# Kernel tuning notes

Hardware: AMD Instinct MI355X
Metric: run time of the kernel (lower is better)

## Reference

```python
import jax, jax.numpy as jnp
import numpy as np

HEAD_SIZE = 128

def setup_inputs() -> dict:
    key = jax.random.key(0)
    ks = jax.random.split(key, 4)
    B, T, C, H = 8, 2048, 1024, HEAD_SIZE
    x = jax.random.normal(ks[0], (B, T, C), dtype=jnp.float32)
    Wk = jax.random.normal(ks[1], (C, H), dtype=jnp.float32) * (C ** -0.5)
    Wq = jax.random.normal(ks[2], (C, H), dtype=jnp.float32) * (C ** -0.5)
    Wv = jax.random.normal(ks[3], (C, H), dtype=jnp.float32) * (C ** -0.5)
    return {"x": x, "Wk": Wk, "Wq": Wq, "Wv": Wv}

def reference(x, Wk, Wq, Wv):
    # x: [B,T,C]; projections to [B,T,H]
    k = jnp.einsum('btc,ch->bth', x, Wk)
    q = jnp.einsum('btc,ch->bth', x, Wq)
    v = jnp.einsum('btc,ch->bth', x, Wv)
    scale = HEAD_SIZE ** -0.5
    wei = jnp.einsum('bqh,bkh->bqk', q, k) * scale  # [B,T,T]
    T = x.shape[1]
    causal = jnp.tril(jnp.ones((T, T), dtype=bool))
    wei = jnp.where(causal, wei, -jnp.inf)
    wei = jax.nn.softmax(wei, axis=-1)
    # dropout p=0 (eval) -> identity
    out = jnp.einsum('bqk,bkh->bqh', wei, v)  # [B,T,H]
    return out
```

## Files before the change

### kernel.cpp

```cpp
#include <hip/hip_runtime.h>

#define B_DIM 8
#define T_DIM 2048
#define C_DIM 1024
#define H_DIM 128

typedef __attribute__((ext_vector_type(8))) short bf16x8;
typedef __attribute__((ext_vector_type(4))) float f32x4;

__device__ __forceinline__ short f2bf(float f) {
  union { float f; unsigned u; } v; v.f = f;
  unsigned u = v.u;
  unsigned r = (u + 0x7FFFu + ((u >> 16) & 1u)) >> 16;
  return (short)r;
}

__device__ __forceinline__ void gload_lds16(const short* g, short* l) {
  __builtin_amdgcn_global_load_lds(
      (const __attribute__((address_space(1))) void*)g,
      (__attribute__((address_space(3))) void*)l, 16, 0, 0);
}

__device__ __forceinline__ float rowmax16(float x) {
  union { float f; int i; } a, t;
  a.f = x;
  t.i = __builtin_amdgcn_update_dpp(a.i, a.i, 0x128, 0xf, 0xf, false);
  a.f = fmaxf(a.f, t.f);
  t.i = __builtin_amdgcn_update_dpp(a.i, a.i, 0x124, 0xf, 0xf, false);
  a.f = fmaxf(a.f, t.f);
  t.i = __builtin_amdgcn_update_dpp(a.i, a.i, 0x122, 0xf, 0xf, false);
  a.f = fmaxf(a.f, t.f);
  t.i = __builtin_amdgcn_update_dpp(a.i, a.i, 0x121, 0xf, 0xf, false);
  a.f = fmaxf(a.f, t.f);
  return a.f;
}
__device__ __forceinline__ float rowsum16(float x) {
  union { float f; int i; } a, t;
  a.f = x;
  t.i = __builtin_amdgcn_update_dpp(a.i, a.i, 0x128, 0xf, 0xf, false);
  a.f += t.f;
  t.i = __builtin_amdgcn_update_dpp(a.i, a.i, 0x124, 0xf, 0xf, false);
  a.f += t.f;
  t.i = __builtin_amdgcn_update_dpp(a.i, a.i, 0x122, 0xf, 0xf, false);
  a.f += t.f;
  t.i = __builtin_amdgcn_update_dpp(a.i, a.i, 0x121, 0xf, 0xf, false);
  a.f += t.f;
  return a.f;
}

#define NWE ((3 * C_DIM * H_DIM) / 8)

__global__ __launch_bounds__(256) void wprep_kernel(
    const float* __restrict__ Wk, const float* __restrict__ Wq,
    const float* __restrict__ Wv, short* __restrict__ Wt) {
  int j = blockIdx.x * 256 + threadIdx.x;
  if (j >= NWE) return;
  int w = j >> 14;
  int r = j & 16383;
  int h = r >> 7;
  int c0 = (r & 127) * 8;
  const float* W = (w == 0) ? Wk : ((w == 1) ? Wq : Wv);
  __attribute__((aligned(16))) short t[8];
#pragma unroll
  for (int i = 0; i < 8; i++) t[i] = f2bf(W[(size_t)(c0 + i) * H_DIM + h]);
  *(int4*)(Wt + (size_t)w * (C_DIM * H_DIM) + h * C_DIM + c0) = *(const int4*)t;
}

__global__ __launch_bounds__(512, 2) void projf_kernel(
    const float* __restrict__ x, const short* __restrict__ Wt,
    short* __restrict__ Kp, short* __restrict__ Qb, short* __restrict__ Vp) {
  const int m0 = blockIdx.x * 64;
  __shared__ short As[64][72];
  __shared__ short Bs[384 * 64];
  const int tid  = threadIdx.x;
  const int lane = tid & 63;
  const int wv   = tid >> 6;
  const int n    = lane & 15;
  const int quad = lane >> 4;
  const int mh = wv >> 2;
  const int nq = wv & 3;

  const int ar = tid >> 3, ac = (tid & 7) * 8;
  const float* xrow = x + (size_t)(m0 + ar) * C_DIM + ac;
  const int brl = lane >> 3;
  const int bce = 8 * ((lane & 7) ^ brl);

  f32x4 acc[2][6];
#pragma unroll
  for (int i = 0; i < 2; i++)
#pragma unroll
    for (int j = 0; j < 6; j++) {
      f32x4 z = {0.f, 0.f, 0.f, 0.f};
      acc[i][j] = z;
    }

  float4 ax0, ax1;
  auto LOADA = [&](int k0) {
    ax0 = *(const float4*)(xrow + k0);
    ax1 = *(const float4*)(xrow + k0 + 4);
  };
  auto STOREA = [&]() {
    __attribute__((aligned(16))) short t8[8];
    t8[0] = f2bf(ax0.x); t8[1] = f2bf(ax0.y); t8[2] = f2bf(ax0.z); t8[3] = f2bf(ax0.w);
    t8[4] = f2bf(ax1.x); t8[5] = f2bf(ax1.y); t8[6] = f2bf(ax1.z); t8[7] = f2bf(ax1.w);
    *(int4*)&As[ar][ac] = *(const int4*)t8;
  };

  LOADA(0);
  for (int it = 0; it < 16; it++) {
    const int k0 = it * 64;
    __syncthreads();
#pragma unroll
    for (int h = 0; h < 6; h++) {
      int c = wv * 6 + h;
      gload_lds16(Wt + (size_t)(c * 8 + brl) * C_DIM + k0 + bce, &Bs[c * 512]);
    }
    STOREA();
    if (it < 15) LOADA(k0 + 64);
    __syncthreads();

#pragma unroll
    for (int kk = 0; kk < 2; kk++) {
      bf16x8 aF[2], bF[6];
#pragma unroll
      for (int mt = 0; mt < 2; mt++)
        aF[mt] = *(const bf16x8*)&As[mh * 32 + mt * 16 + n][kk * 32 + quad * 8];
#pragma unroll
      for (int nt = 0; nt < 6; nt++) {
        int row = nq * 96 + nt * 16 + n;
        int off = (kk * 64 + quad * 16) ^ ((row & 7) << 4);
        bF[nt] = *(const bf16x8*)((const char*)&Bs[row * 64] + off);
      }
#pragma unroll
      for (int mt = 0; mt < 2; mt++)
#pragma unroll
        for (int nt = 0; nt < 6; nt++)
          acc[mt][nt] = __builtin_amdgcn_mfma_f32_16x16x32_bf16(
              aF[mt], bF[nt], acc[mt][nt], 0, 0, 0);
    }
  }

#pragma unroll
  for (int mt = 0; mt < 2; mt++) {
#pragma unroll
    for (int nt = 0; nt < 6; nt++) {
#pragma unroll
      for (int i = 0; i < 4; i++) {
        int row = m0 + mh * 32 + mt * 16 + quad * 4 + i;
        int col = nq * 96 + nt * 16 + n;
        short v = f2bf(acc[mt][nt][i]);
        int w = col >> 7;
        int c = col & 127;
        int bb = row >> 11;
        int t  = row & (T_DIM - 1);
        int tt = t >> 6;
        if (w == 0) {
          int rr = t & 63;
          int knt = rr >> 4, kn = rr & 15;
          int kc = c >> 5, kq = (c >> 3) & 3, kj = c & 7;
          Kp[(((size_t)(bb * 32 + tt) * 16 + knt * 4 + kc) * 512) +
             (kq * 16 + kn) * 8 + kj] = v;
        } else if (w == 1) {
          Qb[(size_t)row * H_DIM + c] = v;
        } else {
          int vkc = (t >> 5) & 1, vq = (t >> 3) & 3, vj = t & 7;
          int ht = c >> 4, vn = c & 15;
          Vp[(((size_t)(bb * 32 + tt) * 16 + ht * 2 + vkc) * 512) +
             (vq * 16 + vn) * 8 + vj] = v;
        }
      }
    }
  }
}

__global__ __launch_bounds__(256, 2) void attn_kernel(
    const short* __restrict__ Qb, const short* __restrict__ Kp,
    const short* __restrict__ Vp, float* __restrict__ out) {
  const int id = blockIdx.y * 128 + blockIdx.x;
  const int b  = id & 7;
  const int qt = 127 - (id >> 3);
  const int q0 = qt * 16;
  const int tid  = threadIdx.x;
  const int lane = tid & 63;
  const int g    = tid >> 6;
  const int n    = lane & 15;
  const int quad = lane >> 4;

  __shared__ short Ps[4][16][72];
  __shared__ float Om[16][128];
  __shared__ float Ml[16][2];

  const int ntiles = (qt >> 2) + 1;
  const float scale = 0.08838834764831845f;
  const int row0 = q0 + quad * 4;

  const short* Kbase = Kp + (size_t)b * 32 * 16 * 512;
  const short* Vbase = Vp + (size_t)b * 32 * 16 * 512;

  bf16x8 aQ[4];
  {
    const short* qrow = Qb + (size_t)(b * T_DIM + q0 + n) * H_DIM;
#pragma unroll
    for (int kc = 0; kc < 4; kc++)
      aQ[kc] = *(const bf16x8*)(qrow + kc * 32 + quad * 8);
  }

  f32x4 accO[8];
#pragma unroll
  for (int i = 0; i < 8; i++) {
    f32x4 z = {0.f, 0.f, 0.f, 0.f};
    accO[i] = z;
  }
  float mrow[4] = {-1e30f, -1e30f, -1e30f, -1e30f};
  float lrow[4] = {0.f, 0.f, 0.f, 0.f};

  for (int t = g; t < ntiles; t += 4) {
    const int j0 = t * 64;
    const short* Kt = Kbase + (size_t)t * 16 * 512 + lane * 8;
    const short* Vt = Vbase + (size_t)t * 16 * 512 + lane * 8;
    f32x4 accS[4];
#pragma unroll
    for (int nt = 0; nt < 4; nt++) {
      f32x4 z = {0.f, 0.f, 0.f, 0.f};
      accS[nt] = z;
    }
    bf16x8 fr[16];
#pragma unroll
    for (int nt = 0; nt < 4; nt++)
#pragma unroll
      for (int kc = 0; kc < 4; kc++)
        fr[nt * 4 + kc] = *(const bf16x8*)(Kt + (nt * 4 + kc) * 512);
    __builtin_amdgcn_sched_barrier(0);
#pragma unroll
    for (int nt = 0; nt < 4; nt++)
#pragma unroll
      for (int kc = 0; kc < 4; kc++)
        accS[nt] = __builtin_amdgcn_mfma_f32_16x16x32_bf16(
            aQ[kc], fr[nt * 4 + kc], accS[nt], 0, 0, 0);
    __builtin_amdgcn_sched_barrier(0);

    float mt4[4] = {-1e30f, -1e30f, -1e30f, -1e30f};
#pragma unroll
    for (int nt = 0; nt < 4; nt++) {
      int col = j0 + nt * 16 + n;
#pragma unroll
      for (int i = 0; i < 4; i++) {
        float s = accS[nt][i] * scale;
        s = (col > row0 + i) ? -1e30f : s;
        accS[nt][i] = s;
        mt4[i] = fmaxf(mt4[i], s);
      }
    }
#pragma unroll
    for (int i = 0; i < 4; i++) mt4[i] = rowmax16(mt4[i]);

    bf16x8 frv[8];
#pragma unroll
    for (int ht = 0; ht < 4; ht++)
#pragma unroll
      for (int kc = 0; kc < 2; kc++)
        frv[ht * 2 + kc] = *(const bf16x8*)(Vt + (ht * 2 + kc) * 512);
    __builtin_amdgcn_sched_barrier(0);

    float alpha[4], rsum[4];
#pragma unroll
    for (int i = 0; i < 4; i++) {
      float mnew = fmaxf(mrow[i], mt4[i]);
      alpha[i] = __expf(mrow[i] - mnew);
      mrow[i] = mnew;
      rsum[i] = 0.f;
    }
#pragma unroll
    for (int nt = 0; nt < 4; nt++)
#pragma unroll
      for (int i = 0; i < 4; i++) {
        float p = __expf(accS[nt][i] - mrow[i]);
        rsum[i] += p;
        Ps[g][quad * 4 + i][nt * 16 + n] = f2bf(p);
      }
#pragma unroll
    for (int i = 0; i < 4; i++) {
      rsum[i] = rowsum16(rsum[i]);
      lrow[i] = lrow[i] * alpha[i] + rsum[i];
    }
#pragma unroll
    for (int ht = 0; ht < 8; ht++)
#pragma unroll
      for (int i = 0; i < 4; i++)
        accO[ht][i] *= alpha[i];

    asm volatile("s_waitcnt lgkmcnt(0)" ::: "memory");
    __builtin_amdgcn_sched_barrier(0);

    bf16x8 aP[2];
#pragma unroll
    for (int kc = 0; kc < 2; kc++)
      aP[kc] = *(const bf16x8*)&Ps[g][n][kc * 32 + quad * 8];

#pragma unroll
    for (int ht = 0; ht < 4; ht++)
#pragma unroll
      for (int kc = 0; kc < 2; kc++)
        accO[ht] = __builtin_amdgcn_mfma_f32_16x16x32_bf16(
            aP[kc], frv[ht * 2 + kc], accO[ht], 0, 0, 0);
    __builtin_amdgcn_sched_barrier(0);
#pragma unroll
    for (int ht = 0; ht < 4; ht++)
#pragma unroll
      for (int kc = 0; kc < 2; kc++)
        frv[ht * 2 + kc] = *(const bf16x8*)(Vt + ((ht + 4) * 2 + kc) * 512);
    __builtin_amdgcn_sched_barrier(0);
#pragma unroll
    for (int ht = 0; ht < 4; ht++)
#pragma unroll
      for (int kc = 0; kc < 2; kc++)
        accO[ht + 4] = __builtin_amdgcn_mfma_f32_16x16x32_bf16(
            aP[kc], frv[ht * 2 + kc], accO[ht + 4], 0, 0, 0);
  }

  __syncthreads();
  if (g == 0) {
#pragma unroll
    for (int i = 0; i < 4; i++) {
      int r = quad * 4 + i;
#pragma unroll
      for (int ht = 0; ht < 8; ht++)
        Om[r][ht * 16 + n] = accO[ht][i];
      if (n == 0) { Ml[r][0] = mrow[i]; Ml[r][1] = lrow[i]; }
    }
  }
#pragma unroll
  for (int gg = 1; gg < 4; gg++) {
    __syncthreads();
    if (g == gg) {
#pragma unroll
      for (int i = 0; i < 4; i++) {
        int r = quad * 4 + i;
        float m1 = Ml[r][0], l1 = Ml[r][1];
        float mnew = fmaxf(mrow[i], m1);
        float a0 = __expf(mrow[i] - mnew);
        float a1 = __expf(m1 - mnew);
        float lnew = lrow[i] * a0 + l1 * a1;
        if (gg < 3) {
          if (n == 0) { Ml[r][0] = mnew; Ml[r][1] = lnew; }
#pragma unroll
          for (int ht = 0; ht < 8; ht++)
            Om[r][ht * 16 + n] = accO[ht][i] * a0 + Om[r][ht * 16 + n] * a1;
        } else {
          float linv = 1.0f / lnew;
          size_t base = (size_t)(b * T_DIM + q0 + r) * H_DIM;
#pragma unroll
          for (int ht = 0; ht < 8; ht++)
            out[base + ht * 16 + n] =
                (accO[ht][i] * a0 + Om[r][ht * 16 + n] * a1) * linv;
        }
      }
    }
  }
}

extern "C" void kernel_launch(void* const* d_in, const int* in_sizes, int n_in,
                              void* d_out, int out_size, void* d_ws, size_t ws_size,
                              hipStream_t stream) {
  (void)in_sizes; (void)n_in; (void)out_size; (void)ws_size;
  const float* x  = (const float*)d_in[0];
  const float* Wk = (const float*)d_in[1];
  const float* Wq = (const float*)d_in[2];
  const float* Wv = (const float*)d_in[3];
  float* out = (float*)d_out;

  char* ws = (char*)d_ws;
  short* Wt = (short*)ws;
  short* Kp = (short*)(ws + 786432);
  short* Qb = (short*)(ws + 786432 + 4194304);
  short* Vp = (short*)(ws + 786432 + 8388608);

  wprep_kernel<<<dim3(192), dim3(256), 0, stream>>>(Wk, Wq, Wv, Wt);
  projf_kernel<<<dim3(256), dim3(512), 0, stream>>>(x, Wt, Kp, Qb, Vp);
  attn_kernel<<<dim3(128, 8), dim3(256), 0, stream>>>(Qb, Kp, Vp, out);
}
```

Measured before the change: 159.9 us.

## Double-buffer projection GEMM LDS tiles with explicit waitcnt pipelining

Gives the QKV projection kernel two LDS buffers for A and B and restructures the K loop so global-to-LDS loads of the tile two steps ahead are issued while the current tile is computed. Explicit vmcnt/lgkmcnt waits and s_barriers replace the plain __syncthreads pairs. The goal is to hide global load latency behind MFMA work. In exchange LDS use doubles to about 110KB per block, which may cut occupancy below the 2 blocks the launch bounds ask for, and the hand-set vmcnt counts are fragile.

```diff
diff --git a/kernel.cpp b/kernel.cpp
--- a/kernel.cpp
+++ b/kernel.cpp
@@ -70,8 +70,8 @@
     const float* __restrict__ x, const short* __restrict__ Wt,
     short* __restrict__ Kp, short* __restrict__ Qb, short* __restrict__ Vp) {
   const int m0 = blockIdx.x * 64;
-  __shared__ short As[64][72];
-  __shared__ short Bs[384 * 64];
+  __shared__ short As[2][64][72];
+  __shared__ short Bs[2][384 * 64];
   const int tid  = threadIdx.x;
   const int lane = tid & 63;
   const int wv   = tid >> 6;
@@ -94,42 +94,38 @@
       acc[i][j] = z;
     }
 
-  float4 ax0, ax1;
-  auto LOADA = [&](int k0) {
-    ax0 = *(const float4*)(xrow + k0);
-    ax1 = *(const float4*)(xrow + k0 + 4);
+  float4 a0x, a0y, a1x, a1y;
+
+  auto LOADA = [&](int k0, float4& u, float4& v) {
+    u = *(const float4*)(xrow + k0);
+    v = *(const float4*)(xrow + k0 + 4);
   };
-  auto STOREA = [&]() {
+  auto STOREA = [&](int buf, const float4& u, const float4& v) {
     __attribute__((aligned(16))) short t8[8];
-    t8[0] = f2bf(ax0.x); t8[1] = f2bf(ax0.y); t8[2] = f2bf(ax0.z); t8[3] = f2bf(ax0.w);
-    t8[4] = f2bf(ax1.x); t8[5] = f2bf(ax1.y); t8[6] = f2bf(ax1.z); t8[7] = f2bf(ax1.w);
-    *(int4*)&As[ar][ac] = *(const int4*)t8;
+    t8[0] = f2bf(u.x); t8[1] = f2bf(u.y); t8[2] = f2bf(u.z); t8[3] = f2bf(u.w);
+    t8[4] = f2bf(v.x); t8[5] = f2bf(v.y); t8[6] = f2bf(v.z); t8[7] = f2bf(v.w);
+    *(int4*)&As[buf][ar][ac] = *(const int4*)t8;
   };
-
-  LOADA(0);
-  for (int it = 0; it < 16; it++) {
-    const int k0 = it * 64;
-    __syncthreads();
+  auto ISSUEB = [&](int buf, int k0) {
 #pragma unroll
     for (int h = 0; h < 6; h++) {
       int c = wv * 6 + h;
-      gload_lds16(Wt + (size_t)(c * 8 + brl) * C_DIM + k0 + bce, &Bs[c * 512]);
-    }
-    STOREA();
-    if (it < 15) LOADA(k0 + 64);
-    __syncthreads();
-
+      gload_lds16(Wt + (size_t)(c * 8 + brl) * C_DIM + k0 + bce,
+                  &Bs[buf][c * 512]);
+    }
+  };
+  auto COMPUTE = [&](int buf) {
 #pragma unroll
     for (int kk = 0; kk < 2; kk++) {
       bf16x8 aF[2], bF[6];
 #pragma unroll
       for (int mt = 0; mt < 2; mt++)
-        aF[mt] = *(const bf16x8*)&As[mh * 32 + mt * 16 + n][kk * 32 + quad * 8];
+        aF[mt] = *(const bf16x8*)&As[buf][mh * 32 + mt * 16 + n][kk * 32 + quad * 8];
 #pragma unroll
       for (int nt = 0; nt < 6; nt++) {
         int row = nq * 96 + nt * 16 + n;
         int off = (kk * 64 + quad * 16) ^ ((row & 7) << 4);
-        bF[nt] = *(const bf16x8*)((const char*)&Bs[row * 64] + off);
+        bF[nt] = *(const bf16x8*)((const char*)&Bs[buf][row * 64] + off);
       }
 #pragma unroll
       for (int mt = 0; mt < 2; mt++)
@@ -137,6 +133,40 @@
         for (int nt = 0; nt < 6; nt++)
           acc[mt][nt] = __builtin_amdgcn_mfma_f32_16x16x32_bf16(
               aF[mt], bF[nt], acc[mt][nt], 0, 0, 0);
+    }
+  };
+
+  LOADA(0, a0x, a0y);
+  ISSUEB(0, 0);
+  STOREA(0, a0x, a0y);
+  LOADA(64, a1x, a1y);
+  ISSUEB(1, 64);
+  asm volatile("s_waitcnt vmcnt(7)" ::: "memory");
+  asm volatile("s_waitcnt lgkmcnt(0)" ::: "memory");
+  __builtin_amdgcn_sched_barrier(0);
+  __builtin_amdgcn_s_barrier();
+  __builtin_amdgcn_sched_barrier(0);
+
+#pragma unroll
+  for (int t = 0; t < 16; ++t) {
+    COMPUTE(t & 1);
+    if (t < 15) {
+      __builtin_amdgcn_s_barrier();
+      __builtin_amdgcn_sched_barrier(0);
+      if ((t & 1) == 0) STOREA(1, a1x, a1y);
+      else              STOREA(0, a0x, a0y);
+      if (t + 2 < 16) {
+        if ((t & 1) == 0) LOADA((t + 2) * 64, a0x, a0y);
+        else              LOADA((t + 2) * 64, a1x, a1y);
+        ISSUEB(t & 1, (t + 2) * 64);
+        asm volatile("s_waitcnt vmcnt(7)" ::: "memory");
+      } else {
+        asm volatile("s_waitcnt vmcnt(0)" ::: "memory");
+      }
+      asm volatile("s_waitcnt lgkmcnt(0)" ::: "memory");
+      __builtin_amdgcn_sched_barrier(0);
+      __builtin_amdgcn_s_barrier();
+      __builtin_amdgcn_sched_barrier(0);
     }
   }
 
```

Result: no change. 158.1 us (-1.1%).

## Pre-swizzle weights into MFMA fragment layout and read B directly from global

Applied to the files above, without the earlier changes.

The weight prep kernel now writes the bf16 weights in the exact per-lane MFMA fragment order, so the projection kernel loads B fragments straight from global/L2 into registers instead of staging them through LDS. The projection tile shrinks to 32 rows, which doubles the grid to 512 blocks, and the x tile is double-buffered in LDS with register prefetch. This is meant to cut LDS traffic and barriers and to raise parallelism. The trade-off is that each block re-reads the full weight matrix from L2 with no LDS reuse across waves.

```diff
diff --git a/kernel.cpp b/kernel.cpp
--- a/kernel.cpp
+++ b/kernel.cpp
@@ -13,12 +13,6 @@
   unsigned u = v.u;
   unsigned r = (u + 0x7FFFu + ((u >> 16) & 1u)) >> 16;
   return (short)r;
-}
-
-__device__ __forceinline__ void gload_lds16(const short* g, short* l) {
-  __builtin_amdgcn_global_load_lds(
-      (const __attribute__((address_space(1))) void*)g,
-      (__attribute__((address_space(3))) void*)l, 16, 0, 0);
 }
 
 __device__ __forceinline__ float rowmax16(float x) {
@@ -52,7 +46,7 @@
 
 __global__ __launch_bounds__(256) void wprep_kernel(
     const float* __restrict__ Wk, const float* __restrict__ Wq,
-    const float* __restrict__ Wv, short* __restrict__ Wt) {
+    const float* __restrict__ Wv, short* __restrict__ Wtp) {
   int j = blockIdx.x * 256 + threadIdx.x;
   if (j >= NWE) return;
   int w = j >> 14;
@@ -63,92 +57,94 @@
   __attribute__((aligned(16))) short t[8];
 #pragma unroll
   for (int i = 0; i < 8; i++) t[i] = f2bf(W[(size_t)(c0 + i) * H_DIM + h]);
-  *(int4*)(Wt + (size_t)w * (C_DIM * H_DIM) + h * C_DIM + c0) = *(const int4*)t;
+  int colg = w * 128 + h;
+  int nt = colg >> 4, nn = colg & 15;
+  int kc = c0 >> 5, quad = (c0 >> 3) & 3;
+  *(int4*)(Wtp + ((size_t)(nt * 32 + kc) * 64 + quad * 16 + nn) * 8) =
+      *(const int4*)t;
 }
 
 __global__ __launch_bounds__(512, 2) void projf_kernel(
-    const float* __restrict__ x, const short* __restrict__ Wt,
+    const float* __restrict__ x, const short* __restrict__ Wtp,
     short* __restrict__ Kp, short* __restrict__ Qb, short* __restrict__ Vp) {
-  const int m0 = blockIdx.x * 64;
-  __shared__ short As[64][72];
-  __shared__ short Bs[384 * 64];
+  const int m0 = blockIdx.x * 32;
+  __shared__ short As[2][32][72];
   const int tid  = threadIdx.x;
   const int lane = tid & 63;
   const int wv   = tid >> 6;
   const int n    = lane & 15;
   const int quad = lane >> 4;
-  const int mh = wv >> 2;
-  const int nq = wv & 3;
-
-  const int ar = tid >> 3, ac = (tid & 7) * 8;
-  const float* xrow = x + (size_t)(m0 + ar) * C_DIM + ac;
-  const int brl = lane >> 3;
-  const int bce = 8 * ((lane & 7) ^ brl);
-
-  f32x4 acc[2][6];
+
+  const int ar = tid >> 4, ac4 = (tid & 15) * 4;
+  const float* xrow = x + (size_t)(m0 + ar) * C_DIM + ac4;
+  const short* Bw = Wtp + (size_t)(wv * 3) * 32 * 512 + lane * 8;
+
+  f32x4 acc[2][3];
 #pragma unroll
   for (int i = 0; i < 2; i++)
 #pragma unroll
-    for (int j = 0; j < 6; j++) {
+    for (int j = 0; j < 3; j++) {
       f32x4 z = {0.f, 0.f, 0.f, 0.f};
       acc[i][j] = z;
     }
 
-  float4 ax0, ax1;
-  auto LOADA = [&](int k0) {
-    ax0 = *(const float4*)(xrow + k0);
-    ax1 = *(const float4*)(xrow + k0 + 4);
+  float4 s0, s1;
+  auto LOADA = [&](int it, float4& s) { s = *(const float4*)(xrow + it * 64); };
+  auto STOREA = [&](int buf, const float4& s) {
+    __attribute__((aligned(8))) short t4[4];
+    t4[0] = f2bf(s.x); t4[1] = f2bf(s.y); t4[2] = f2bf(s.z); t4[3] = f2bf(s.w);
+    *(int2*)&As[buf][ar][ac4] = *(const int2*)t4;
   };
-  auto STOREA = [&]() {
-    __attribute__((aligned(16))) short t8[8];
-    t8[0] = f2bf(ax0.x); t8[1] = f2bf(ax0.y); t8[2] = f2bf(ax0.z); t8[3] = f2bf(ax0.w);
-    t8[4] = f2bf(ax1.x); t8[5] = f2bf(ax1.y); t8[6] = f2bf(ax1.z); t8[7] = f2bf(ax1.w);
-    *(int4*)&As[ar][ac] = *(const int4*)t8;
-  };
-
-  LOADA(0);
-  for (int it = 0; it < 16; it++) {
-    const int k0 = it * 64;
-    __syncthreads();
-#pragma unroll
-    for (int h = 0; h < 6; h++) {
-      int c = wv * 6 + h;
-      gload_lds16(Wt + (size_t)(c * 8 + brl) * C_DIM + k0 + bce, &Bs[c * 512]);
-    }
-    STOREA();
-    if (it < 15) LOADA(k0 + 64);
-    __syncthreads();
-
-#pragma unroll
-    for (int kk = 0; kk < 2; kk++) {
-      bf16x8 aF[2], bF[6];
-#pragma unroll
-      for (int mt = 0; mt < 2; mt++)
-        aF[mt] = *(const bf16x8*)&As[mh * 32 + mt * 16 + n][kk * 32 + quad * 8];
-#pragma unroll
-      for (int nt = 0; nt < 6; nt++) {
-        int row = nq * 96 + nt * 16 + n;
-        int off = (kk * 64 + quad * 16) ^ ((row & 7) << 4);
-        bF[nt] = *(const bf16x8*)((const char*)&Bs[row * 64] + off);
-      }
-#pragma unroll
-      for (int mt = 0; mt < 2; mt++)
-#pragma unroll
-        for (int nt = 0; nt < 6; nt++)
-          acc[mt][nt] = __builtin_amdgcn_mfma_f32_16x16x32_bf16(
-              aF[mt], bF[nt], acc[mt][nt], 0, 0, 0);
+
+  LOADA(0, s0);
+  STOREA(0, s0);
+  LOADA(1, s1);
+  __syncthreads();
+
+#pragma unroll 2
+  for (int it = 0; it < 16; ++it) {
+    bf16x8 bF[6], aF[4];
+#pragma unroll
+    for (int ntl = 0; ntl < 3; ntl++)
+#pragma unroll
+      for (int kk = 0; kk < 2; kk++)
+        bF[ntl * 2 + kk] =
+            *(const bf16x8*)(Bw + (size_t)(ntl * 32 + it * 2 + kk) * 512);
+#pragma unroll
+    for (int mt = 0; mt < 2; mt++)
+#pragma unroll
+      for (int kk = 0; kk < 2; kk++)
+        aF[mt * 2 + kk] =
+            *(const bf16x8*)&As[it & 1][mt * 16 + n][kk * 32 + quad * 8];
+    __builtin_amdgcn_sched_barrier(0);
+#pragma unroll
+    for (int mt = 0; mt < 2; mt++)
+#pragma unroll
+      for (int ntl = 0; ntl < 3; ntl++)
+#pragma unroll
+        for (int kk = 0; kk < 2; kk++)
+          acc[mt][ntl] = __builtin_amdgcn_mfma_f32_16x16x32_bf16(
+              aF[mt * 2 + kk], bF[ntl * 2 + kk], acc[mt][ntl], 0, 0, 0);
+
+    if (it < 15) {
+      __syncthreads();
+      if (((it + 1) & 1) == 0) STOREA(0, s0); else STOREA(1, s1);
+      if (it + 2 < 16) {
+        if (((it + 2) & 1) == 0) LOADA(it + 2, s0); else LOADA(it + 2, s1);
+      }
+      __syncthreads();
     }
   }
 
 #pragma unroll
   for (int mt = 0; mt < 2; mt++) {
 #pragma unroll
-    for (int nt = 0; nt < 6; nt++) {
+    for (int ntl = 0; ntl < 3; ntl++) {
 #pragma unroll
       for (int i = 0; i < 4; i++) {
-        int row = m0 + mh * 32 + mt * 16 + quad * 4 + i;
-        int col = nq * 96 + nt * 16 + n;
-        short v = f2bf(acc[mt][nt][i]);
+        int row = m0 + mt * 16 + quad * 4 + i;
+        int col = wv * 48 + ntl * 16 + n;
+        short v = f2bf(acc[mt][ntl][i]);
         int w = col >> 7;
         int c = col & 127;
         int bb = row >> 11;
@@ -370,12 +366,12 @@
   float* out = (float*)d_out;
 
   char* ws = (char*)d_ws;
-  short* Wt = (short*)ws;
+  short* Wtp = (short*)ws;
   short* Kp = (short*)(ws + 786432);
   short* Qb = (short*)(ws + 786432 + 4194304);
   short* Vp = (short*)(ws + 786432 + 8388608);
 
-  wprep_kernel<<<dim3(192), dim3(256), 0, stream>>>(Wk, Wq, Wv, Wt);
-  projf_kernel<<<dim3(256), dim3(512), 0, stream>>>(x, Wt, Kp, Qb, Vp);
+  wprep_kernel<<<dim3(192), dim3(256), 0, stream>>>(Wk, Wq, Wv, Wtp);
+  projf_kernel<<<dim3(512), dim3(512), 0, stream>>>(x, Wtp, Kp, Qb, Vp);
   attn_kernel<<<dim3(128, 8), dim3(256), 0, stream>>>(Qb, Kp, Vp, out);
 }
```

Measured after the change: 151.1 us. -5.5%, faster.
